# Kernel optimization log

Measured on AMD Instinct MI355X. Metric: run time of the kernel, lower is better.

The kernel has to match this reference:

```python
import jax, jax.numpy as jnp
import numpy as np

NUM_NODES = 100000
INPUT_DIM = 256
NUM_BAGS = 2048
BAG_SIZE = 64
N_EDGES = 3200000  # num_nodes * avg_degree(32)


def setup_inputs() -> dict:
    key = jax.random.key(0)
    ks = jax.random.split(key, 7)
    x = jax.random.normal(ks[0], (NUM_NODES, INPUT_DIM), dtype=jnp.float32)
    bags = jax.random.randint(ks[1], (NUM_BAGS, BAG_SIZE), 0, NUM_NODES)
    alpha_values = jax.random.uniform(ks[2], (NUM_BAGS, BAG_SIZE, 1), dtype=jnp.float32)
    # edge_dict in COO form: edge_src[e] has neighbor edge_nbr[e]
    edge_src = jax.random.randint(ks[3], (N_EDGES,), 0, NUM_NODES)
    edge_nbr = jax.random.randint(ks[4], (N_EDGES,), 0, NUM_NODES)
    node_weights = jax.random.uniform(ks[5], (NUM_NODES,), dtype=jnp.float32)  # torch.rand init
    theta_w = jax.random.normal(ks[6], (INPUT_DIM,), dtype=jnp.float32) / np.sqrt(INPUT_DIM)
    return dict(x=x, bags=bags, alpha_values=alpha_values, edge_src=edge_src,
                edge_nbr=edge_nbr, node_weights=node_weights, theta_w=theta_w)


def reference(x, bags, alpha_values, edge_src, edge_nbr, node_weights, theta_w):
    # Per-source neighbor weight sum: sum_value(source) = sum(node_weights[edge_dict[source]])
    nbr_sum = jax.ops.segment_sum(node_weights[edge_nbr], edge_src, num_segments=NUM_NODES)
    deg = jax.ops.segment_sum(jnp.ones_like(edge_src, dtype=x.dtype), edge_src,
                              num_segments=NUM_NODES)
    # sources not in edge_dict get sum_value = 1.0
    nbr_sum = jnp.where(deg > 0, nbr_sum, jnp.asarray(1.0, x.dtype))
    # h_values = theta(x[bag]); theta is Linear(input_dim, 1, bias=False)
    h = jnp.einsum('nbd,d->nb', x[bags], theta_w)          # [num_bags, bag_size]
    feat = h * alpha_values[..., 0]                         # [num_bags, bag_size]
    ns = nbr_sum[bags]                                      # [num_bags, bag_size]
    return jnp.sum(ns * feat, axis=1)                       # [num_bags]
```

## Files before the change

kernel.cpp:

```cpp
#include <hip/hip_runtime.h>

#define NUM_NODES 100000
#define INPUT_DIM 256
#define NUM_BAGS  2048
#define BAG_SIZE  64
#define N_EDGES   3200000
#define P_PART    8
#define NPP       12500
#define NSLICE    32

__global__ void __launch_bounds__(1024)
edge_hist(const int* __restrict__ edge_src, const int* __restrict__ edge_nbr,
          const float* __restrict__ nw,
          float* __restrict__ rep,
          unsigned int* __restrict__ deg) {
    __shared__ float hist[NPP];
    const int i    = blockIdx.x;
    const int r    = i & 7;
    const int p    = (i >> 3) & 7;
    const int b    = r | ((i >> 6) << 3);
    const int base = p * NPP;

    for (int j = threadIdx.x; j < NPP; j += 1024) hist[j] = 0.f;
    __syncthreads();

    const int per = (N_EDGES / 4) / NSLICE;
    const int lo  = b * per;
    const int hi  = lo + per;
    for (int q = lo + (int)threadIdx.x; q < hi; q += 1024) {
        const int4 s4 = ((const int4*)edge_src)[q];
        const int4 n4 = ((const int4*)edge_nbr)[q];
#define EDGE(S, N)                                                   \
        {                                                            \
            const unsigned rel = (unsigned)((S) - base);             \
            if (rel < (unsigned)NPP) {                               \
                atomicAdd(&hist[rel], nw[(N)]);      \
                deg[(S)] = 1u;                      \
            }                                                        \
        }
        EDGE(s4.x, n4.x)
        EDGE(s4.y, n4.y)
        EDGE(s4.z, n4.z)
        EDGE(s4.w, n4.w)
#undef EDGE
    }
    __syncthreads();

    float* dst = rep + (size_t)b * NUM_NODES + base;
    for (int j = threadIdx.x; j < NPP; j += 1024) dst[j] = hist[j];
}

__global__ void __launch_bounds__(256)
reduce_rep(const float* __restrict__ rep, const unsigned int* __restrict__ deg,
           float* __restrict__ nbr_sum) {
    const int i = blockIdx.x * 256 + threadIdx.x;
    if (i >= NUM_NODES / 4) return;
    float4 a = make_float4(0.f, 0.f, 0.f, 0.f);
    for (int r = 0; r < NSLICE; ++r) {
        const float4 v = ((const float4*)(rep + (size_t)r * NUM_NODES))[i];
        a.x += v.x; a.y += v.y; a.z += v.z; a.w += v.w;
    }
    const uint4 d = ((const uint4*)deg)[i];
    float4 o;
    o.x = d.x ? a.x : 1.0f;
    o.y = d.y ? a.y : 1.0f;
    o.z = d.z ? a.z : 1.0f;
    o.w = d.w ? a.w : 1.0f;
    ((float4*)nbr_sum)[i] = o;
}

__global__ void __launch_bounds__(256)
gemv_h(const float* __restrict__ x, const float* __restrict__ theta,
       float* __restrict__ h) {
    const int lane = threadIdx.x & 63;
    const int wave = threadIdx.x >> 6;
    const float4 tw = *reinterpret_cast<const float4*>(&theta[lane * 4]);
    const int stride = gridDim.x * 4;
    for (int row = blockIdx.x * 4 + wave; row < NUM_NODES; row += stride) {
        const float4 xv =
            *reinterpret_cast<const float4*>(&x[(size_t)row * INPUT_DIM + lane * 4]);
        float d = xv.x * tw.x + xv.y * tw.y + xv.z * tw.z + xv.w * tw.w;
        #pragma unroll
        for (int off = 32; off >= 1; off >>= 1)
            d += __shfl_xor(d, off);
        if (lane == 0) h[row] = d;
    }
}

__global__ void __launch_bounds__(256)
bag_final(const int* __restrict__ bags, const float* __restrict__ alpha,
          const float* __restrict__ h, const float* __restrict__ ns,
          float* __restrict__ out) {
    const int bag  = blockIdx.x * 4 + (threadIdx.x >> 6);
    const int lane = threadIdx.x & 63;
    const int idx  = bags[bag * BAG_SIZE + lane];
    float v = h[idx] * ns[idx] * alpha[bag * BAG_SIZE + lane];
    #pragma unroll
    for (int off = 32; off >= 1; off >>= 1)
        v += __shfl_xor(v, off);
    if (lane == 0) out[bag] = v;
}

__global__ void __launch_bounds__(256)
edge_atomic(const int* __restrict__ edge_src, const int* __restrict__ edge_nbr,
            const float* __restrict__ nw,
            float* __restrict__ nbr_sum, unsigned int* __restrict__ deg) {
    const int t = blockIdx.x * blockDim.x + threadIdx.x;
    const int4 s4 = ((const int4*)edge_src)[t];
    const int4 n4 = ((const int4*)edge_nbr)[t];
    atomicAdd(&nbr_sum[s4.x], nw[n4.x]);
    atomicAdd(&nbr_sum[s4.y], nw[n4.y]);
    atomicAdd(&nbr_sum[s4.z], nw[n4.z]);
    atomicAdd(&nbr_sum[s4.w], nw[n4.w]);
    deg[s4.x] = 1u; deg[s4.y] = 1u; deg[s4.z] = 1u; deg[s4.w] = 1u;
}

__global__ void __launch_bounds__(256)
fixup_nosum(float* __restrict__ nbr_sum, const unsigned int* __restrict__ deg) {
    const int i = blockIdx.x * 256 + threadIdx.x;
    if (i < NUM_NODES && deg[i] == 0u) nbr_sum[i] = 1.0f;
}

extern "C" void kernel_launch(void* const* d_in, const int* in_sizes, int n_in,
                              void* d_out, int out_size, void* d_ws, size_t ws_size,
                              hipStream_t stream) {
    const float* x            = (const float*)d_in[0];
    const int*   bags         = (const int*)d_in[1];
    const float* alpha        = (const float*)d_in[2];
    const int*   edge_src     = (const int*)d_in[3];
    const int*   edge_nbr     = (const int*)d_in[4];
    const float* node_weights = (const float*)d_in[5];
    const float* theta        = (const float*)d_in[6];
    float*       out          = (float*)d_out;

    const size_t need_full =
        ((size_t)NSLICE * NUM_NODES + 3 * (size_t)NUM_NODES) * 4;

    if (ws_size >= need_full) {
        float*        rep     = (float*)d_ws;
        unsigned int* deg     = (unsigned int*)d_ws + (size_t)NSLICE * NUM_NODES;
        float*        nbr_sum = (float*)deg + NUM_NODES;
        float*        h       = nbr_sum + NUM_NODES;

        hipMemsetAsync(deg, 0, (size_t)NUM_NODES * 4, stream);
        edge_hist<<<P_PART * NSLICE, 1024, 0, stream>>>(edge_src, edge_nbr,
                                                        node_weights, rep, deg);
        gemv_h<<<2048, 256, 0, stream>>>(x, theta, h);
        reduce_rep<<<(NUM_NODES / 4 + 255) / 256, 256, 0, stream>>>(rep, deg,
                                                                    nbr_sum);
        bag_final<<<NUM_BAGS / 4, 256, 0, stream>>>(bags, alpha, h, nbr_sum, out);
    } else {
        float*        nbr_sum = (float*)d_ws;
        unsigned int* deg     = (unsigned int*)d_ws + NUM_NODES;
        float*        h       = (float*)deg + NUM_NODES;
        hipMemsetAsync(d_ws, 0, (size_t)NUM_NODES * 2 * 4, stream);
        edge_atomic<<<(N_EDGES / 4) / 256, 256, 0, stream>>>(
            edge_src, edge_nbr, node_weights, nbr_sum, deg);
        fixup_nosum<<<(NUM_NODES + 255) / 256, 256, 0, stream>>>(nbr_sum, deg);
        gemv_h<<<2048, 256, 0, stream>>>(x, theta, h);
        bag_final<<<NUM_BAGS / 4, 256, 0, stream>>>(bags, alpha, h, nbr_sum, out);
    }
}
```

Before: 76.35 us.

## Fuse edge histogram and GEMV into one launch to overlap their work

Merges the edge histogram kernel and the x·theta GEMV into a single launch. The first 256 blocks build the per-partition histograms and the remaining 128 blocks compute h, so the latency-bound atomic work runs alongside the bandwidth-bound GEMV instead of one after the other. Nontemporal loads and stores are added for the streamed x reads and the replica writes. The trade-off is a fixed GEMV block count and the GEMV blocks sharing the launch's 50KB shared-memory footprint, which may limit occupancy.

Result: slower. 85.46 us (+11.9%).

```diff
diff --git a/kernel.cpp b/kernel.cpp
--- a/kernel.cpp
+++ b/kernel.cpp
@@ -8,46 +8,70 @@
 #define P_PART    8
 #define NPP       12500
 #define NSLICE    32
+#define EDGE_BLOCKS (P_PART * NSLICE)
+#define GEMV_BLOCKS 128
+
+typedef float f4_t __attribute__((ext_vector_type(4)));
 
 __global__ void __launch_bounds__(1024)
-edge_hist(const int* __restrict__ edge_src, const int* __restrict__ edge_nbr,
-          const float* __restrict__ nw,
-          float* __restrict__ rep,
-          unsigned int* __restrict__ deg) {
+fused_edge_gemv(const int* __restrict__ edge_src, const int* __restrict__ edge_nbr,
+                const float* __restrict__ nw,
+                float* __restrict__ rep,
+                unsigned int* __restrict__ deg,
+                const float* __restrict__ x, const float* __restrict__ theta,
+                float* __restrict__ h) {
     __shared__ float hist[NPP];
-    const int i    = blockIdx.x;
-    const int r    = i & 7;
-    const int p    = (i >> 3) & 7;
-    const int b    = r | ((i >> 6) << 3);
-    const int base = p * NPP;
 
-    for (int j = threadIdx.x; j < NPP; j += 1024) hist[j] = 0.f;
-    __syncthreads();
+    if (blockIdx.x < EDGE_BLOCKS) {
+        const int i    = blockIdx.x;
+        const int r    = i & 7;
+        const int p    = (i >> 3) & 7;
+        const int b    = r | ((i >> 6) << 3);
+        const int base = p * NPP;
 
-    const int per = (N_EDGES / 4) / NSLICE;
-    const int lo  = b * per;
-    const int hi  = lo + per;
-    for (int q = lo + (int)threadIdx.x; q < hi; q += 1024) {
-        const int4 s4 = ((const int4*)edge_src)[q];
-        const int4 n4 = ((const int4*)edge_nbr)[q];
-#define EDGE(S, N)                                                   \
-        {                                                            \
-            const unsigned rel = (unsigned)((S) - base);             \
-            if (rel < (unsigned)NPP) {                               \
-                atomicAdd(&hist[rel], nw[(N)]);      \
-                deg[(S)] = 1u;                      \
-            }                                                        \
+        for (int j = threadIdx.x; j < NPP; j += 1024) hist[j] = 0.f;
+        __syncthreads();
+
+        const int per = (N_EDGES / 4) / NSLICE;
+        const int lo  = b * per;
+        const int hi  = lo + per;
+        for (int q = lo + (int)threadIdx.x; q < hi; q += 1024) {
+            const int4 s4 = ((const int4*)edge_src)[q];
+            const int4 n4 = ((const int4*)edge_nbr)[q];
+#define EDGE(S, N)                                                     \
+            {                                                          \
+                const unsigned rel = (unsigned)((S) - base);           \
+                if (rel < (unsigned)NPP) {                             \
+                    atomicAdd(&hist[rel], nw[(N)]);    \
+                    deg[(S)] = 1u;                                     \
+                }                                                      \
+            }
+            EDGE(s4.x, n4.x)
+            EDGE(s4.y, n4.y)
+            EDGE(s4.z, n4.z)
+            EDGE(s4.w, n4.w)
+#undef EDGE
         }
-        EDGE(s4.x, n4.x)
-        EDGE(s4.y, n4.y)
-        EDGE(s4.z, n4.z)
-        EDGE(s4.w, n4.w)
-#undef EDGE
+        __syncthreads();
+
+        float* dst = rep + (size_t)b * NUM_NODES + base;
+        for (int j = threadIdx.x; j < NPP; j += 1024)
+            __builtin_nontemporal_store(hist[j], &dst[j]);
+    } else {
+        const int gb   = blockIdx.x - EDGE_BLOCKS;
+        const int lane = threadIdx.x & 63;
+        const int wave = threadIdx.x >> 6;
+        const f4_t tw  = *(const f4_t*)&theta[lane * 4];
+        for (int row = gb * 16 + wave; row < NUM_NODES; row += GEMV_BLOCKS * 16) {
+            const f4_t xv = __builtin_nontemporal_load(
+                (const f4_t*)&x[(size_t)row * INPUT_DIM + lane * 4]);
+            float d = xv.x * tw.x + xv.y * tw.y + xv.z * tw.z + xv.w * tw.w;
+            #pragma unroll
+            for (int off = 32; off >= 1; off >>= 1)
+                d += __shfl_xor(d, off);
+            if (lane == 0) h[row] = d;
+        }
     }
-    __syncthreads();
-
-    float* dst = rep + (size_t)b * NUM_NODES + base;
-    for (int j = threadIdx.x; j < NPP; j += 1024) dst[j] = hist[j];
 }
 
 __global__ void __launch_bounds__(256)
@@ -67,24 +91,6 @@
     o.z = d.z ? a.z : 1.0f;
     o.w = d.w ? a.w : 1.0f;
     ((float4*)nbr_sum)[i] = o;
-}
-
-__global__ void __launch_bounds__(256)
-gemv_h(const float* __restrict__ x, const float* __restrict__ theta,
-       float* __restrict__ h) {
-    const int lane = threadIdx.x & 63;
-    const int wave = threadIdx.x >> 6;
-    const float4 tw = *reinterpret_cast<const float4*>(&theta[lane * 4]);
-    const int stride = gridDim.x * 4;
-    for (int row = blockIdx.x * 4 + wave; row < NUM_NODES; row += stride) {
-        const float4 xv =
-            *reinterpret_cast<const float4*>(&x[(size_t)row * INPUT_DIM + lane * 4]);
-        float d = xv.x * tw.x + xv.y * tw.y + xv.z * tw.z + xv.w * tw.w;
-        #pragma unroll
-        for (int off = 32; off >= 1; off >>= 1)
-            d += __shfl_xor(d, off);
-        if (lane == 0) h[row] = d;
-    }
 }
 
 __global__ void __launch_bounds__(256)
@@ -121,6 +127,24 @@
     if (i < NUM_NODES && deg[i] == 0u) nbr_sum[i] = 1.0f;
 }
 
+__global__ void __launch_bounds__(256)
+gemv_h(const float* __restrict__ x, const float* __restrict__ theta,
+       float* __restrict__ h) {
+    const int lane = threadIdx.x & 63;
+    const int wave = threadIdx.x >> 6;
+    const float4 tw = *reinterpret_cast<const float4*>(&theta[lane * 4]);
+    const int stride = gridDim.x * 4;
+    for (int row = blockIdx.x * 4 + wave; row < NUM_NODES; row += stride) {
+        const float4 xv =
+            *reinterpret_cast<const float4*>(&x[(size_t)row * INPUT_DIM + lane * 4]);
+        float d = xv.x * tw.x + xv.y * tw.y + xv.z * tw.z + xv.w * tw.w;
+        #pragma unroll
+        for (int off = 32; off >= 1; off >>= 1)
+            d += __shfl_xor(d, off);
+        if (lane == 0) h[row] = d;
+    }
+}
+
 extern "C" void kernel_launch(void* const* d_in, const int* in_sizes, int n_in,
                               void* d_out, int out_size, void* d_ws, size_t ws_size,
                               hipStream_t stream) {
@@ -143,9 +167,8 @@
         float*        h       = nbr_sum + NUM_NODES;
 
         hipMemsetAsync(deg, 0, (size_t)NUM_NODES * 4, stream);
-        edge_hist<<<P_PART * NSLICE, 1024, 0, stream>>>(edge_src, edge_nbr,
-                                                        node_weights, rep, deg);
-        gemv_h<<<2048, 256, 0, stream>>>(x, theta, h);
+        fused_edge_gemv<<<EDGE_BLOCKS + GEMV_BLOCKS, 1024, 0, stream>>>(
+            edge_src, edge_nbr, node_weights, rep, deg, x, theta, h);
         reduce_rep<<<(NUM_NODES / 4 + 255) / 256, 256, 0, stream>>>(rep, deg,
                                                                     nbr_sum);
         bag_final<<<NUM_BAGS / 4, 256, 0, stream>>>(bags, alpha, h, nbr_sum, out);
```
